# Kernel optimization log

Measured on AMD Instinct MI355X. Metric: run time of the kernel, lower is better.

Reference implementation:

```python
import jax, jax.numpy as jnp
import numpy as np

DIM = 384; KEY_DIM = 32; HEADS = 8; ATTN_RATIO = 4; RES = 14
D = ATTN_RATIO * KEY_DIM          # 128
DH = D * HEADS                    # 1024
QK = HEADS * KEY_DIM              # 256
B = 64
EPS = 1e-5
SCALE = KEY_DIM ** -0.5


def _bn(x, p):
    # inference-mode BatchNorm; p = [gamma, beta, mean, var] each [C]; channel axis = 1
    g, b, m, v = p
    shp = (1, -1) + (1,) * (x.ndim - 2)
    return (x - m.reshape(shp)) * jax.lax.rsqrt(v.reshape(shp) + EPS) * g.reshape(shp) + b.reshape(shp)


def _bn_params(k, c):
    k1, k2, k3, k4 = jax.random.split(k, 4)
    gamma = 1.0 + 0.1 * jax.random.normal(k1, (c,), dtype=jnp.float32)
    beta = 0.02 * jax.random.normal(k2, (c,), dtype=jnp.float32)
    mean = 0.1 * jax.random.normal(k3, (c,), dtype=jnp.float32)
    var = jax.random.uniform(k4, (c,), dtype=jnp.float32) + 0.5
    return jnp.stack([gamma, beta, mean, var])


def setup_inputs() -> dict:
    key = jax.random.key(0)
    ks = jax.random.split(key, 24)
    def rn(i, shape, s=0.05):
        return s * jax.random.normal(ks[i], shape, dtype=jnp.float32)
    # relative-position bias index table: offset (|dy|,|dx|) -> dy*RES+dx
    coords = np.stack(np.meshgrid(np.arange(RES), np.arange(RES), indexing='ij'), -1).reshape(-1, 2)
    off = np.abs(coords[:, None, :] - coords[None, :, :])  # [N,N,2]
    bias_idxs = jnp.asarray(off[..., 0] * RES + off[..., 1], dtype=jnp.int32)  # [N,N]
    return {
        'x': jax.random.normal(ks[0], (B, DIM, RES, RES), dtype=jnp.float32),
        'wq': rn(1, (QK, DIM)), 'bq': rn(2, (QK,)), 'bnq': _bn_params(ks[3], QK),
        'wk': rn(4, (QK, DIM)), 'bk': rn(5, (QK,)), 'bnk': _bn_params(ks[6], QK),
        'wv': rn(7, (DH, DIM)), 'bv': rn(8, (DH,)), 'bnv': _bn_params(ks[9], DH),
        'wvl': rn(10, (DH, 1, 3, 3)), 'bvl': rn(11, (DH,)), 'bnvl': _bn_params(ks[12], DH),
        'th1w': rn(13, (HEADS, HEADS), 0.2), 'th1b': rn(14, (HEADS,)),
        'th2w': rn(15, (HEADS, HEADS), 0.2), 'th2b': rn(16, (HEADS,)),
        'wp': rn(17, (DIM, DH)), 'bp': rn(18, (DIM,)), 'bnp': _bn_params(ks[19], DIM),
        'ab': rn(20, (HEADS, RES * RES), 0.1),
        'bias_idxs': bias_idxs,
    }


def reference(x, wq, bq, bnq, wk, bk, bnk, wv, bv, bnv, wvl, bvl, bnvl,
              th1w, th1b, th2w, th2b, wp, bp, bnp, ab, bias_idxs):
    Bn, C, H, W = x.shape
    N = H * W
    xf = x.reshape(Bn, C, N)
    # 1x1 conv + BN branches (channel GEMMs)
    q = _bn(jnp.einsum('oc,bcn->bon', wq, xf) + bq[None, :, None], bnq)
    k = _bn(jnp.einsum('oc,bcn->bon', wk, xf) + bk[None, :, None], bnk)
    v = _bn(jnp.einsum('oc,bcn->bon', wv, xf) + bv[None, :, None], bnv)  # [B,DH,N]
    # local value path: 3x3 depthwise conv + BN
    v_img = v.reshape(Bn, DH, H, W)
    v_local = jax.lax.conv_general_dilated(
        v_img, wvl, window_strides=(1, 1), padding='SAME',
        feature_group_count=DH, dimension_numbers=('NCHW', 'OIHW', 'NCHW'))
    v_local = _bn(v_local + bvl[None, :, None, None], bnvl)
    # attention
    qh = q.reshape(Bn, HEADS, KEY_DIM, N).transpose(0, 1, 3, 2)  # b h n d
    kh = k.reshape(Bn, HEADS, KEY_DIM, N)                        # b h d m
    vh = v.reshape(Bn, HEADS, D, N).transpose(0, 1, 3, 2)        # b h m e
    attn = jnp.einsum('bhnd,bhdm->bhnm', qh, kh) * SCALE
    attn = attn + ab[:, bias_idxs][None]                         # [1,H,N,N] positional bias
    attn = jnp.einsum('oh,bhnm->bonm', th1w, attn) + th1b[None, :, None, None]
    attn = jax.nn.softmax(attn, axis=-1)
    attn = jnp.einsum('oh,bhnm->bonm', th2w, attn) + th2b[None, :, None, None]
    out = jnp.einsum('bhnm,bhme->bhne', attn, vh)                # b h n e
    out = out.transpose(0, 1, 3, 2).reshape(Bn, DH, H, W) + v_local
    # proj: ReLU -> 1x1 conv -> BN
    out = jax.nn.relu(out)
    out = jnp.einsum('oc,bchw->bohw', wp, out) + bp[None, :, None, None]
    return _bn(out, bnp)
```

## Files before the change

### kernel.cpp

```cpp
#include <hip/hip_runtime.h>

#define B_     64
#define DIM_   384
#define RES_   14
#define N_     196
#define HEADS_ 8
#define KD_    32
#define D_     128
#define DH_    1024
#define QK_    256
#define CH_    1536
#define EPS_   1e-5f
#define SCALE_ 0.17677669529663687f

typedef unsigned short u16;
typedef unsigned int u32;
typedef short v8s __attribute__((ext_vector_type(8)));
typedef float v4f __attribute__((ext_vector_type(4)));
typedef u16  v4u __attribute__((ext_vector_type(4)));

static __device__ __forceinline__ u16 f2bf(float f) {
    unsigned int u = __builtin_bit_cast(unsigned int, f);
    u = (u + 0x7fffu + ((u >> 16) & 1u)) >> 16;
    return (u16)u;
}
static __device__ __forceinline__ float bf2f(u16 u) {
    unsigned int x = ((unsigned int)u) << 16;
    return __builtin_bit_cast(float, x);
}
static __device__ __forceinline__ u16 f2h(float f) {
    _Float16 h = (_Float16)f;
    return __builtin_bit_cast(u16, h);
}
static __device__ __forceinline__ float h2f(u16 u) {
    return (float)__builtin_bit_cast(_Float16, u);
}

#define WBI_OFF  0u
#define WPI_OFF  589824u
#define QI_OFF   983040u
#define KI_OFF   5177344u
#define VI_OFF   9371648u
#define VLOC_U16 53411840u
#define TAIL_OFF 79101952u
#define TB_OFF   98770944u
#define BIASE_OFF 98785920u

template<int KSTEPS>
static __device__ __forceinline__ void gemm_direct(
    const u16* __restrict__ Ag, const u16* __restrict__ Bg,
    v4f acc[4][4], int tid)
{
    const int lane = tid & 63, w = tid >> 6;
    const int wm = (w & 1) * 64, wn = (w >> 1) * 64;
    const int quad = lane >> 4, l16 = lane & 15;
    const u16* pa = Ag + quad * 1024 + (wm + l16) * 8;
    const u16* pb = Bg + quad * 1024 + (wn + l16) * 8;
    v8s a[2][4], b[2][4];
    #pragma unroll
    for (int i = 0; i < 4; i++) {
        a[0][i] = *(const v8s*)(pa + i * 128);
        b[0][i] = *(const v8s*)(pb + i * 128);
    }
    #pragma unroll
    for (int ks = 0; ks < KSTEPS; ks++) {
        const int cur = ks & 1, nxt = cur ^ 1;
        if (ks + 1 < KSTEPS) {
            const u16* qa = pa + (size_t)(ks + 1) * 4096;
            const u16* qb = pb + (size_t)(ks + 1) * 4096;
            #pragma unroll
            for (int i = 0; i < 4; i++) {
                a[nxt][i] = *(const v8s*)(qa + i * 128);
                b[nxt][i] = *(const v8s*)(qb + i * 128);
            }
        }
        #pragma unroll
        for (int i = 0; i < 4; i++)
            #pragma unroll
            for (int j = 0; j < 4; j++)
                acc[i][j] = __builtin_amdgcn_mfma_f32_16x16x32_bf16(a[cur][i], b[cur][j], acc[i][j], 0, 0, 0);
    }
}

template<int KSTEPS>
static __device__ __forceinline__ void gemm_direct3(
    const u16* __restrict__ Ag, const u16* __restrict__ Bg,
    v4f acc[4][4], int tid)
{
    const int lane = tid & 63, w = tid >> 6;
    const int wm = (w & 1) * 64, wn = (w >> 1) * 64;
    const int quad = lane >> 4, l16 = lane & 15;
    const u16* pa = Ag + quad * 1024 + (wm + l16) * 8;
    const u16* pb = Bg + quad * 1024 + (wn + l16) * 8;
    v8s a[3][4], b[3][4];
    #pragma unroll
    for (int s = 0; s < 2; s++) {
        #pragma unroll
        for (int i = 0; i < 4; i++) {
            a[s][i] = *(const v8s*)(pa + (size_t)s * 4096 + i * 128);
            b[s][i] = *(const v8s*)(pb + (size_t)s * 4096 + i * 128);
        }
    }
    #pragma unroll
    for (int ks = 0; ks < KSTEPS; ks++) {
        const int cur = ks % 3, nxt = (ks + 2) % 3;
        if (ks + 2 < KSTEPS) {
            const u16* qa = pa + (size_t)(ks + 2) * 4096;
            const u16* qb = pb + (size_t)(ks + 2) * 4096;
            #pragma unroll
            for (int i = 0; i < 4; i++) {
                a[nxt][i] = *(const v8s*)(qa + i * 128);
                b[nxt][i] = *(const v8s*)(qb + i * 128);
            }
        }
        #pragma unroll
        for (int i = 0; i < 4; i++)
            #pragma unroll
            for (int j = 0; j < 4; j++)
                acc[i][j] = __builtin_amdgcn_mfma_f32_16x16x32_bf16(a[cur][i], b[cur][j], acc[i][j], 0, 0, 0);
    }
}

__global__ __launch_bounds__(256) void k_pre(
    const float* __restrict__ x,
    const float* __restrict__ wq, const float* __restrict__ wk,
    const float* __restrict__ wv, const float* __restrict__ wp,
    const float* __restrict__ ab,
    const float* __restrict__ th1w, const float* __restrict__ th1b,
    const float* __restrict__ bq, const float* __restrict__ bnq,
    const float* __restrict__ bk, const float* __restrict__ bnk,
    const float* __restrict__ bv, const float* __restrict__ bnv,
    const float* __restrict__ bp, const float* __restrict__ bnp,
    const float* __restrict__ bvl, const float* __restrict__ bnvl,
    const int* __restrict__ bidx,
    u16* __restrict__ xI, u16* __restrict__ WbI, u16* __restrict__ WpI,
    float* __restrict__ TB, float* __restrict__ biasE)
{
    __shared__ float T[64][65];
    const int tid = threadIdx.x;
    if (blockIdx.x < 1536) {
        const int t  = blockIdx.x;
        const int n0 = (t & 3) * 64;
        const int k0 = ((t >> 2) % 6) * 64;
        const int b  = t / 24;
        const int c = tid & 63, r4 = tid >> 6;
        #pragma unroll
        for (int i = 0; i < 16; i++) {
            int kr = i * 4 + r4;
            int gn = n0 + c;
            T[kr][c] = (gn < N_) ? x[((size_t)b * DIM_ + k0 + kr) * N_ + gn] : 0.f;
        }
        __syncthreads();
        #pragma unroll
        for (int it = 0; it < 16; it++) {
            int j = it * 256 + tid;
            int kk = j & 63, nn = j >> 6;
            int k = k0 + kk, n = n0 + nn;
            xI[(size_t)b * 98304 + (n >> 7) * 49152 + (k >> 5) * 4096
               + ((k >> 3) & 3) * 1024 + (n & 127) * 8 + (k & 7)] = f2bf(T[kk][nn]);
        }
        return;
    }
    int i = (blockIdx.x - 1536) * 256 + tid;
    if (i < 589824) {
        int mt = i / 49152, rem = i % 49152;
        int ks = rem >> 12, r2 = rem & 4095;
        int q = r2 >> 10, row = (r2 >> 3) & 127, e = r2 & 7;
        int c = mt * 128 + row, k = ks * 32 + q * 8 + e;
        float v = (c < 256) ? wq[c * 384 + k]
                : (c < 512) ? wk[(c - 256) * 384 + k]
                            : wv[(size_t)(c - 512) * 384 + k];
        WbI[i] = f2bf(v);
    } else if (i < 983040) {
        int j = i - 589824;
        int mt = j >> 17, rem = j & 131071;
        int ks = rem >> 12, r2 = rem & 4095;
        int q = r2 >> 10, row = (r2 >> 3) & 127, e = r2 & 7;
        int p = mt * 128 + row, k = ks * 32 + q * 8 + e;
        WpI[j] = f2bf(wp[(size_t)p * 1024 + k]);
    } else if (i < 985984) {
        int j = i - 983040;
        if (j < 256) {
            int c = j;
            float s = bnq[c] * rsqrtf(bnq[768 + c] + EPS_);
            float t = (bq[c] - bnq[512 + c]) * s + bnq[256 + c];
            TB[c] = s * SCALE_; TB[256 + c] = t * SCALE_;
        } else if (j < 512) {
            int c = j - 256;
            float s = bnk[c] * rsqrtf(bnk[768 + c] + EPS_);
            float t = (bk[c] - bnk[512 + c]) * s + bnk[256 + c];
            TB[512 + c] = s; TB[768 + c] = t;
        } else if (j < 1536) {
            int c = j - 512;
            float s = bnv[c] * rsqrtf(bnv[3072 + c] + EPS_);
            float t = (bv[c] - bnv[2048 + c]) * s + bnv[1024 + c];
            TB[1024 + c] = s; TB[2048 + c] = t;
        } else if (j < 1920) {
            int c = j - 1536;
            float s = bnp[c] * rsqrtf(bnp[1152 + c] + EPS_);
            float t = (bp[c] - bnp[768 + c]) * s + bnp[384 + c];
            TB[3072 + c] = s; TB[3456 + c] = t;
        } else {
            int c = j - 1920;
            float s = bnvl[c] * rsqrtf(bnvl[3072 + c] + EPS_);
            float t = (bvl[c] - bnvl[2048 + c]) * s + bnvl[1024 + c];
            TB[3840 + c] = s; TB[4864 + c] = t;
        }
    } else if (i < 1293312) {
        int j = i - 985984;
        int m = j % N_;
        int t = j / N_;
        int o = t & 7;
        int n = t >> 3;
        int idx = bidx[n * N_ + m];
        float a = th1b[o];
        #pragma unroll
        for (int h = 0; h < 8; h++) a += th1w[o * 8 + h] * ab[h * N_ + idx];
        biasE[j] = a - 5.f;
    }
}

__global__ __launch_bounds__(256) void k_qkv(
    const u16* __restrict__ WbI, const u16* __restrict__ xI,
    const float* __restrict__ TB,
    u16* __restrict__ qI, u16* __restrict__ kI, u16* __restrict__ vI)
{
    const int tid = threadIdx.x;
    const int L = blockIdx.x + 2 * (blockIdx.y + 12 * blockIdx.z);
    const int idx = L >> 3;
    const int b  = (L & 7) * 8 + idx / 24;
    const int r  = idx % 24;
    const int mt = r >> 1, nt = r & 1;
    v4f acc[4][4] = {};
    gemm_direct<12>(WbI + (size_t)mt * 49152,
                    xI + ((size_t)b * 2 + nt) * 49152, acc, tid);

    const int lane = tid & 63, w = tid >> 6;
    const int wm = (w & 1) * 64, wn = (w >> 1) * 64;
    const int quad = lane >> 4, l16 = lane & 15;
    #pragma unroll
    for (int i = 0; i < 4; i++) {
        #pragma unroll
        for (int j = 0; j < 4; j++) {
            int gc = mt * 128 + wm + i * 16 + quad * 4;
            int n  = nt * 128 + wn + j * 16 + l16;
            v4f v = acc[i][j];
            if (gc < 256) {
                v4f s = *(const v4f*)&TB[gc];
                v4f t = *(const v4f*)&TB[256 + gc];
                v4u u;
                #pragma unroll
                for (int r2 = 0; r2 < 4; r2++) u[r2] = f2bf(v[r2] * s[r2] + t[r2]);
                *(v4u*)&qI[((size_t)(b * 8 + (gc >> 5)) * 256 + n) * 32 + (gc & 31)] = u;
            } else if (gc < 512) {
                int c = gc - 256;
                v4f s = *(const v4f*)&TB[512 + c];
                v4f t = *(const v4f*)&TB[768 + c];
                v4u u;
                #pragma unroll
                for (int r2 = 0; r2 < 4; r2++) u[r2] = f2bf(v[r2] * s[r2] + t[r2]);
                *(v4u*)&kI[((size_t)(b * 8 + (c >> 5)) * 256 + n) * 32 + (c & 31)] = u;
            } else {
                int c = gc - 512;
                if (n < 224) {
                    int o = c >> 7, e = c & 127;
                    u16* base = vI + ((size_t)(b * 8 + o) * 7 + (n >> 5)) * 4096
                                + ((n >> 3) & 3) * 1024 + (n & 7);
                    #pragma unroll
                    for (int r2 = 0; r2 < 4; r2++) {
                        u16 outv = 0;
                        if (n < N_) outv = f2bf(v[r2] * TB[1024 + c + r2] + TB[2048 + c + r2]);
                        base[(e + r2) * 8] = outv;
                    }
                }
            }
        }
    }
}

__global__ __launch_bounds__(256) void k_dwconv(
    const u16* __restrict__ vI, const float* __restrict__ wvl,
    const float* __restrict__ TB, u16* __restrict__ vlocI)
{
    __shared__ u16 V[64 * 230];
    const int tid = threadIdx.x;
    const int sub = blockIdx.x;
    const int b   = blockIdx.y;
    const int o   = sub >> 1;
    const int e0  = (sub & 1) * 64;
    const u16* img = vI + (size_t)(b * 8 + o) * 28672;

    {
        const int quad = tid >> 6, l = tid & 63;
        #pragma unroll
        for (int i = 0; i < 7; i++) {
            v8s u = *(const v8s*)&img[i * 4096 + quad * 1024 + (e0 + l) * 8];
            const u32* ui = (const u32*)&u;
            int m0 = i * 32 + quad * 8;
            u32* dst = (u32*)&V[l * 230 + m0];
            #pragma unroll
            for (int c = 0; c < 4; c++) dst[c] = ui[c];
        }
    }
    __syncthreads();

    const int e = tid & 63, j = tid >> 6;
    const int cg = sub * 64 + e;
    const int y0 = j * 4;
    const int ny = (j == 3) ? 2 : 4;
    float wgt[9];
    #pragma unroll
    for (int k = 0; k < 9; k++) wgt[k] = wvl[cg * 9 + k];
    const float sc = TB[3840 + cg], sh = TB[4864 + cg];
    u32 po[4][7];

    for (int yi = 0; yi < ny; yi++) {
        int y = y0 + yi;
        float a[3][16];
        #pragma unroll
        for (int dy = 0; dy < 3; dy++) {
            int yy = y + dy - 1;
            a[dy][0] = 0.f; a[dy][15] = 0.f;
            if (yy < 0 || yy > 13) {
                #pragma unroll
                for (int x = 1; x < 15; x++) a[dy][x] = 0.f;
            } else {
                const u16* rp = &V[e * 230 + yy * 14];
                #pragma unroll
                for (int c4 = 0; c4 < 7; c4++) {
                    u32 u = *(const u32*)&rp[c4 * 2];
                    a[dy][1 + 2 * c4] = bf2f((u16)(u & 0xffffu));
                    a[dy][2 + 2 * c4] = bf2f((u16)(u >> 16));
                }
            }
        }
        #pragma unroll
        for (int xp = 0; xp < 7; xp++) {
            u32 pk = 0;
            #pragma unroll
            for (int half = 0; half < 2; half++) {
                int x = 2 * xp + half;
                float s = 0.f;
                #pragma unroll
                for (int dy = 0; dy < 3; dy++)
                    #pragma unroll
                    for (int kx = 0; kx < 3; kx++)
                        s += wgt[dy * 3 + kx] * a[dy][x + kx];
                u16 bv = f2bf(s * sc + sh);
                pk |= ((u32)bv) << (16 * half);
            }
            po[yi][xp] = pk;
        }
    }
    __syncthreads();

    for (int yi = 0; yi < ny; yi++) {
        u32* dst = (u32*)&V[e * 196 + (y0 + yi) * 14];
        #pragma unroll
        for (int xp = 0; xp < 7; xp++) dst[xp] = po[yi][xp];
    }
    __syncthreads();

    for (int it = 0; it < 7; it++) {
        int idx = it * 256 + tid;
        if (idx < 1568) {
            int g = idx / 196, n = idx - g * 196;
            v4u lo, hi;
            #pragma unroll
            for (int r = 0; r < 4; r++) lo[r] = V[(g * 8 + r) * 196 + n];
            #pragma unroll
            for (int r = 0; r < 4; r++) hi[r] = V[(g * 8 + 4 + r) * 196 + n];
            u16* dst = vlocI + ((size_t)(b * 2 + (n >> 7)) * 32 + sub * 2 + (g >> 2)) * 4096
                     + (g & 3) * 1024 + (n & 127) * 8;
            *(v4u*)dst = lo;
            *(v4u*)(dst + 4) = hi;
        }
    }
}

__global__ __launch_bounds__(512) void k_attn_av(
    const u16* __restrict__ qI, const u16* __restrict__ kI,
    const u16* __restrict__ vI,
    const float* __restrict__ th1w,
    const float* __restrict__ th2w, const float* __restrict__ th2b,
    const float* __restrict__ biasE,
    const u16* __restrict__ vlocI, u16* __restrict__ aoI)
{
    __shared__ u16 Sl[8 * 16 * 228];
    __shared__ float red[128][4];
    __shared__ float invS[128];
    const int tid = threadIdx.x;
    const int w = tid >> 6, lane = tid & 63;
    const int quad = lane >> 4, l16 = lane & 15;
    const int L = blockIdx.x + 13 * blockIdx.y;
    const int idx = L >> 3;
    const int b  = (L & 7) * 8 + idx / 13;
    const int qt = idx % 13;
    const int n0 = qt * 16;

    {
        const int h = w;
        const u16* qb = qI + (size_t)(b * 8 + h) * 8192;
        const u16* kb = kI + (size_t)(b * 8 + h) * 8192;
        v8s qf = *(const v8s*)&qb[(n0 + l16) * 32 + quad * 8];
        #pragma unroll
        for (int mt = 0; mt < 13; mt++) {
            v8s kf = *(const v8s*)&kb[(mt * 16 + l16) * 32 + quad * 8];
            v4f acc = {};
            acc = __builtin_amdgcn_mfma_f32_16x16x32_bf16(kf, qf, acc, 0, 0, 0);
            v4u pk;
            #pragma unroll
            for (int r = 0; r < 4; r++) pk[r] = f2h(acc[r]);
            *(v4u*)&Sl[(h * 16 + l16) * 228 + mt * 16 + quad * 4] = pk;
        }
    }
    __syncthreads();

    const int mp  = (tid & 127) * 2;
    const int qh  = tid >> 7;
    const bool pvalid = (mp < N_);
    for (int qq = 0; qq < 4; qq++) {
        int q = qh * 4 + qq;
        int n = n0 + q;
        if (pvalid && n < N_) {
            const float* bE = biasE + (size_t)n * 1568 + mp;
            float S0[8], S1[8];
            #pragma unroll
            for (int h = 0; h < 8; h++) {
                u32 u = *(const u32*)&Sl[(h * 16 + q) * 228 + mp];
                S0[h] = h2f((u16)(u & 0xffffu));
                S1[h] = h2f((u16)(u >> 16));
            }
            u32 ew[8];
            #pragma unroll
            for (int o = 0; o < 8; o++) {
                float2 bb = *(const float2*)&bE[o * 196];
                float a0 = bb.x, a1 = bb.y;
                #pragma unroll
                for (int h = 0; h < 8; h++) {
                    a0 += th1w[o * 8 + h] * S0[h];
                    a1 += th1w[o * 8 + h] * S1[h];
                }
                ew[o] = (u32)f2h(__expf(a0)) | ((u32)f2h(__expf(a1)) << 16);
            }
            #pragma unroll
            for (int o = 0; o < 8; o++)
                *(u32*)&Sl[(o * 16 + q) * 228 + mp] = ew[o];
        }
    }
    __syncthreads();

    {
        int r = tid >> 2, quarter = tid & 3;
        int mstart = quarter * 48;
        int cnt = (quarter == 3) ? 26 : 24;
        const u16* rowp = &Sl[r * 228 + mstart];
        float s = 0.f;
        for (int i = 0; i < cnt; i++) {
            u32 u = *(const u32*)&rowp[i * 2];
            s += h2f((u16)(u & 0xffffu)) + h2f((u16)(u >> 16));
        }
        red[r][quarter] = s;
    }
    __syncthreads();
    if (tid < 128)
        invS[tid] = 1.f / (red[tid][0] + red[tid][1] + red[tid][2] + red[tid][3]);
    __syncthreads();

    for (int qq = 0; qq < 4; qq++) {
        int q = qh * 4 + qq;
        bool valid = pvalid && (n0 + q < N_);
        u32 pw[8];
        if (valid) {
            float s0[8], s1[8];
            #pragma unroll
            for (int h = 0; h < 8; h++) {
                u32 u = *(const u32*)&Sl[(h * 16 + q) * 228 + mp];
                float is = invS[h * 16 + q];
                s0[h] = h2f((u16)(u & 0xffffu)) * is;
                s1[h] = h2f((u16)(u >> 16)) * is;
            }
            #pragma unroll
            for (int o = 0; o < 8; o++) {
                float v0 = th2b[o], v1 = th2b[o];
                #pragma unroll
                for (int h = 0; h < 8; h++) {
                    v0 += th2w[o * 8 + h] * s0[h];
                    v1 += th2w[o * 8 + h] * s1[h];
                }
                pw[o] = (u32)f2bf(v0) | ((u32)f2bf(v1) << 16);
            }
        } else {
            #pragma unroll
            for (int o = 0; o < 8; o++) pw[o] = 0;
        }
        if (mp < 224) {
            #pragma unroll
            for (int o = 0; o < 8; o++)
                *(u32*)&Sl[(o * 16 + q) * 228 + mp] = pw[o];
        }
    }
    __syncthreads();

    {
        const int half_ = n0 >> 7;
        const int row0 = n0 & 127;
        const int n = n0 + l16;
        const bool act = (n < N_);
        const int o = w;
        const u16* vb = vI + (size_t)(b * 8 + o) * 28672;
        const u16* prow = &Sl[(o * 16 + l16) * 228];
        __builtin_amdgcn_s_setprio(1);
        #pragma unroll
        for (int eh = 0; eh < 2; eh++) {
            v4f acc[4] = {};
            v8s a[2][4];
            const u16* ab0 = vb + quad * 1024 + (eh * 64 + l16) * 8;
            #pragma unroll
            for (int e = 0; e < 4; e++) a[0][e] = *(const v8s*)(ab0 + e * 128);
            #pragma unroll
            for (int ks = 0; ks < 7; ks++) {
                const int cur = ks & 1, nxt = cur ^ 1;
                if (ks < 6) {
                    const u16* an = ab0 + (size_t)(ks + 1) * 4096;
                    #pragma unroll
                    for (int e = 0; e < 4; e++) a[nxt][e] = *(const v8s*)(an + e * 128);
                }
                v8s bfr = *(const v8s*)&prow[ks * 32 + quad * 8];
                #pragma unroll
                for (int e = 0; e < 4; e++)
                    acc[e] = __builtin_amdgcn_mfma_f32_16x16x32_bf16(a[cur][e], bfr, acc[e], 0, 0, 0);
            }
            if (act) {
                #pragma unroll
                for (int e = 0; e < 4; e++) {
                    const int c0 = o * 128 + (eh * 4 + e) * 16 + quad * 4;
                    const size_t ioff = ((size_t)(b * 2 + half_) * 32 + (c0 >> 5)) * 4096
                                      + ((c0 >> 3) & 3) * 1024 + (size_t)(row0 + l16) * 8 + (c0 & 7);
                    v4u lv = *(const v4u*)&vlocI[ioff];
                    v4u u;
                    #pragma unroll
                    for (int r = 0; r < 4; r++)
                        u[r] = f2bf(fmaxf(acc[e][r] + bf2f(lv[r]), 0.f));
                    *(v4u*)&aoI[ioff] = u;
                }
            }
        }
        __builtin_amdgcn_s_setprio(0);
    }
}

__global__ __launch_bounds__(256) void k_proj(
    const u16* __restrict__ WpI, const u16* __restrict__ aoI,
    const float* __restrict__ TB, float* __restrict__ out)
{
    const int tid = threadIdx.x;
    const int L = blockIdx.x + 2 * (blockIdx.y + 3 * blockIdx.z);
    const int idx = L >> 3;
    const int b  = (L & 7) * 8 + idx / 6;
    const int r  = idx % 6;
    const int mt = r >> 1, nt = r & 1;
    v4f acc[4][4] = {};
    gemm_direct3<32>(WpI + (size_t)mt * 131072,
                     aoI + ((size_t)b * 2 + nt) * 131072, acc, tid);

    const int lane = tid & 63, w = tid >> 6;
    const int wm = (w & 1) * 64, wn = (w >> 1) * 64;
    const int quad = lane >> 4, l16 = lane & 15;
    #pragma unroll
    for (int i = 0; i < 4; i++) {
        #pragma unroll
        for (int j = 0; j < 4; j++) {
            int p0 = mt * 128 + wm + i * 16 + quad * 4;
            int n  = nt * 128 + wn + j * 16 + l16;
            if (n < N_) {
                v4f s = *(const v4f*)&TB[3072 + p0];
                v4f t = *(const v4f*)&TB[3456 + p0];
                #pragma unroll
                for (int r2 = 0; r2 < 4; r2++)
                    out[((size_t)b * DIM_ + p0 + r2) * N_ + n] = acc[i][j][r2] * s[r2] + t[r2];
            }
        }
    }
}

extern "C" void kernel_launch(void* const* d_in, const int* in_sizes, int n_in,
                              void* d_out, int out_size, void* d_ws, size_t ws_size,
                              hipStream_t stream)
{
    const float* x    = (const float*)d_in[0];
    const float* wq   = (const float*)d_in[1];
    const float* bq   = (const float*)d_in[2];
    const float* bnq  = (const float*)d_in[3];
    const float* wk   = (const float*)d_in[4];
    const float* bk   = (const float*)d_in[5];
    const float* bnk  = (const float*)d_in[6];
    const float* wv   = (const float*)d_in[7];
    const float* bv   = (const float*)d_in[8];
    const float* bnv  = (const float*)d_in[9];
    const float* wvl  = (const float*)d_in[10];
    const float* bvl  = (const float*)d_in[11];
    const float* bnvl = (const float*)d_in[12];
    const float* th1w = (const float*)d_in[13];
    const float* th1b = (const float*)d_in[14];
    const float* th2w = (const float*)d_in[15];
    const float* th2b = (const float*)d_in[16];
    const float* wp   = (const float*)d_in[17];
    const float* bp   = (const float*)d_in[18];
    const float* bnp  = (const float*)d_in[19];
    const float* ab   = (const float*)d_in[20];
    const int*   bidx = (const int*)d_in[21];
    float* out = (float*)d_out;

    u16* wsb  = (u16*)d_ws;
    u16* WbI  = wsb + WBI_OFF;
    u16* WpI  = wsb + WPI_OFF;
    u16* qI   = wsb + QI_OFF;
    u16* kI   = wsb + KI_OFF;
    u16* vI   = wsb + VI_OFF;
    u16* vlocI = wsb + VLOC_U16;
    u16* xI   = wsb + TAIL_OFF;
    u16* aoI  = wsb + TAIL_OFF;
    float* TB    = (float*)(wsb + TB_OFF);
    float* biasE = (float*)(wsb + BIASE_OFF);

    k_pre<<<dim3(6588), 256, 0, stream>>>(x, wq, wk, wv, wp, ab, th1w, th1b,
                                          bq, bnq, bk, bnk, bv, bnv, bp, bnp, bvl, bnvl,
                                          bidx, xI, WbI, WpI, TB, biasE);
    k_qkv<<<dim3(2, 12, B_), 256, 0, stream>>>(WbI, xI, TB, qI, kI, vI);
    k_dwconv<<<dim3(16, B_), 256, 0, stream>>>(vI, wvl, TB, vlocI);
    k_attn_av<<<dim3(13, B_), 512, 0, stream>>>(qI, kI, vI, th1w, th2w, th2b,
                                                biasE, vlocI, aoI);
    k_proj<<<dim3(2, 3, B_), 256, 0, stream>>>(WpI, aoI, TB, out);
}
```

Before: 251.6 us.

## Keep attention scores in registers across head-mixing and softmax in attn kernel

Restructures the attention+AV kernel so each wave owns key tiles rather than heads. It computes all 8 heads' QK scores in registers, applies the th1 mix and exp there, and reduces row sums with shuffles plus a small shared buffer. The large shared score buffer and its multiple LDS round trips disappear. The th2-mixed probabilities are then staged per output head through a double-buffered small LDS tile, feeding a smaller per-wave AV MFMA. This raises register pressure, adds a barrier per head iteration, and moves the normalization into fp16 multiplies.

```diff
diff --git a/kernel.cpp b/kernel.cpp
--- a/kernel.cpp
+++ b/kernel.cpp
@@ -18,6 +18,8 @@
 typedef short v8s __attribute__((ext_vector_type(8)));
 typedef float v4f __attribute__((ext_vector_type(4)));
 typedef u16  v4u __attribute__((ext_vector_type(4)));
+typedef u32  v2u __attribute__((ext_vector_type(2)));
+typedef _Float16 h2 __attribute__((ext_vector_type(2)));
 
 static __device__ __forceinline__ u16 f2bf(float f) {
     unsigned int u = __builtin_bit_cast(unsigned int, f);
@@ -27,13 +29,6 @@
 static __device__ __forceinline__ float bf2f(u16 u) {
     unsigned int x = ((unsigned int)u) << 16;
     return __builtin_bit_cast(float, x);
-}
-static __device__ __forceinline__ u16 f2h(float f) {
-    _Float16 h = (_Float16)f;
-    return __builtin_bit_cast(u16, h);
-}
-static __device__ __forceinline__ float h2f(u16 u) {
-    return (float)__builtin_bit_cast(_Float16, u);
 }
 
 #define WBI_OFF  0u
@@ -378,7 +373,8 @@
     }
 }
 
-__global__ __launch_bounds__(512) void k_attn_av(
+#define SLST 232
+__global__ __launch_bounds__(512, 4) void k_attn_av(
     const u16* __restrict__ qI, const u16* __restrict__ kI,
     const u16* __restrict__ vI,
     const float* __restrict__ th1w,
@@ -386,9 +382,10 @@
     const float* __restrict__ biasE,
     const u16* __restrict__ vlocI, u16* __restrict__ aoI)
 {
-    __shared__ u16 Sl[8 * 16 * 228];
-    __shared__ float red[128][4];
-    __shared__ float invS[128];
+    __shared__ __attribute__((aligned(16))) u16 Ps[2][16 * SLST];
+    __shared__ float red[8][8][16];
+    __shared__ float invS[8][16];
+    __shared__ __attribute__((aligned(16))) u16 Zf[8];
     const int tid = threadIdx.x;
     const int w = tid >> 6, lane = tid & 63;
     const int quad = lane >> 4, l16 = lane & 15;
@@ -397,156 +394,140 @@
     const int b  = (L & 7) * 8 + idx / 13;
     const int qt = idx % 13;
     const int n0 = qt * 16;
+    if (tid < 8) Zf[tid] = 0;
+
+    const int nmt = (w < 5) ? 2 : 1;
+    const int nq  = n0 + l16;
+    const int nb  = (nq < N_) ? nq : 0;
+    const float* bErow = biasE + (size_t)nb * 1568;
+
+    h2 E[2][8][2] = {};
+    #pragma unroll
+    for (int mi = 0; mi < 2; mi++) {
+        if (mi >= nmt) break;
+        const int mt = w + mi * 8;
+        v4f S[8];
+        const u16* qb0 = qI + (size_t)b * 8 * 8192;
+        const u16* kb0 = kI + (size_t)b * 8 * 8192;
+        #pragma unroll
+        for (int h = 0; h < 8; h++) {
+            v8s qf = *(const v8s*)&qb0[h * 8192 + (n0 + l16) * 32 + quad * 8];
+            v8s kf = *(const v8s*)&kb0[h * 8192 + (mt * 16 + l16) * 32 + quad * 8];
+            v4f z = {};
+            S[h] = __builtin_amdgcn_mfma_f32_16x16x32_bf16(kf, qf, z, 0, 0, 0);
+        }
+        const bool mvalid = (mt < 12) || (quad == 0);
+        const int mb = mt * 16 + quad * 4;
+        if (mvalid) {
+            #pragma unroll
+            for (int o = 0; o < 8; o++) {
+                v4f a = *(const v4f*)&bErow[o * 196 + mb];
+                #pragma unroll
+                for (int h = 0; h < 8; h++) {
+                    float t1 = th1w[o * 8 + h];
+                    #pragma unroll
+                    for (int r = 0; r < 4; r++) a[r] += t1 * S[h][r];
+                }
+                E[mi][o][0] = h2{(_Float16)__expf(a[0]), (_Float16)__expf(a[1])};
+                E[mi][o][1] = h2{(_Float16)__expf(a[2]), (_Float16)__expf(a[3])};
+            }
+        }
+    }
 
     {
-        const int h = w;
-        const u16* qb = qI + (size_t)(b * 8 + h) * 8192;
-        const u16* kb = kI + (size_t)(b * 8 + h) * 8192;
-        v8s qf = *(const v8s*)&qb[(n0 + l16) * 32 + quad * 8];
-        #pragma unroll
-        for (int mt = 0; mt < 13; mt++) {
-            v8s kf = *(const v8s*)&kb[(mt * 16 + l16) * 32 + quad * 8];
-            v4f acc = {};
-            acc = __builtin_amdgcn_mfma_f32_16x16x32_bf16(kf, qf, acc, 0, 0, 0);
-            v4u pk;
-            #pragma unroll
-            for (int r = 0; r < 4; r++) pk[r] = f2h(acc[r]);
-            *(v4u*)&Sl[(h * 16 + l16) * 228 + mt * 16 + quad * 4] = pk;
-        }
+        float psum[8];
+        #pragma unroll
+        for (int o = 0; o < 8; o++) {
+            float s = (float)E[0][o][0].x + (float)E[0][o][0].y
+                    + (float)E[0][o][1].x + (float)E[0][o][1].y
+                    + (float)E[1][o][0].x + (float)E[1][o][0].y
+                    + (float)E[1][o][1].x + (float)E[1][o][1].y;
+            s += __shfl_xor(s, 16, 64);
+            s += __shfl_xor(s, 32, 64);
+            psum[o] = s;
+        }
+        red[w][quad * 2 + 0][l16] = psum[quad * 2 + 0];
+        red[w][quad * 2 + 1][l16] = psum[quad * 2 + 1];
     }
     __syncthreads();
-
-    const int mp  = (tid & 127) * 2;
-    const int qh  = tid >> 7;
-    const bool pvalid = (mp < N_);
-    for (int qq = 0; qq < 4; qq++) {
-        int q = qh * 4 + qq;
-        int n = n0 + q;
-        if (pvalid && n < N_) {
-            const float* bE = biasE + (size_t)n * 1568 + mp;
-            float S0[8], S1[8];
-            #pragma unroll
-            for (int h = 0; h < 8; h++) {
-                u32 u = *(const u32*)&Sl[(h * 16 + q) * 228 + mp];
-                S0[h] = h2f((u16)(u & 0xffffu));
-                S1[h] = h2f((u16)(u >> 16));
-            }
-            u32 ew[8];
-            #pragma unroll
-            for (int o = 0; o < 8; o++) {
-                float2 bb = *(const float2*)&bE[o * 196];
-                float a0 = bb.x, a1 = bb.y;
-                #pragma unroll
-                for (int h = 0; h < 8; h++) {
-                    a0 += th1w[o * 8 + h] * S0[h];
-                    a1 += th1w[o * 8 + h] * S1[h];
+    if (tid < 128) {
+        int o = tid >> 4, q = tid & 15;
+        float s = 0.f;
+        #pragma unroll
+        for (int wv = 0; wv < 8; wv++) s += red[wv][o][q];
+        invS[o][q] = 1.f / s;
+    }
+    __syncthreads();
+
+    #pragma unroll
+    for (int o = 0; o < 8; o++) {
+        float is = invS[o][l16];
+        h2 is2 = h2{(_Float16)is, (_Float16)is};
+        E[0][o][0] *= is2; E[0][o][1] *= is2;
+        E[1][o][0] *= is2; E[1][o][1] *= is2;
+    }
+
+    const int half_ = n0 >> 7;
+    const int row0 = n0 & 127;
+    const bool act = (nq < N_);
+    char* psrow0 = (char*)&Ps[0][0] + l16 * (SLST * 2);
+    char* psrow1 = (char*)&Ps[1][0] + l16 * (SLST * 2);
+
+    #pragma unroll
+    for (int o2 = 0; o2 < 8; o2++) {
+        char* psb = (o2 & 1) ? psrow1 : psrow0;
+        #pragma unroll
+        for (int mi = 0; mi < 2; mi++) {
+            if (mi >= nmt) break;
+            const int mt = w + mi * 8;
+            const bool mvalid = (mt < 12) || (quad == 0);
+            u32 pk0 = 0, pk1 = 0;
+            if (mvalid) {
+                float p0 = th2b[o2], p1 = th2b[o2], p2 = th2b[o2], p3 = th2b[o2];
+                #pragma unroll
+                for (int o = 0; o < 8; o++) {
+                    float wgt = th2w[o2 * 8 + o];
+                    p0 += wgt * (float)E[mi][o][0].x;
+                    p1 += wgt * (float)E[mi][o][0].y;
+                    p2 += wgt * (float)E[mi][o][1].x;
+                    p3 += wgt * (float)E[mi][o][1].y;
                 }
-                ew[o] = (u32)f2h(__expf(a0)) | ((u32)f2h(__expf(a1)) << 16);
-            }
-            #pragma unroll
-            for (int o = 0; o < 8; o++)
-                *(u32*)&Sl[(o * 16 + q) * 228 + mp] = ew[o];
-        }
-    }
-    __syncthreads();
-
-    {
-        int r = tid >> 2, quarter = tid & 3;
-        int mstart = quarter * 48;
-        int cnt = (quarter == 3) ? 26 : 24;
-        const u16* rowp = &Sl[r * 228 + mstart];
-        float s = 0.f;
-        for (int i = 0; i < cnt; i++) {
-            u32 u = *(const u32*)&rowp[i * 2];
-            s += h2f((u16)(u & 0xffffu)) + h2f((u16)(u >> 16));
-        }
-        red[r][quarter] = s;
-    }
-    __syncthreads();
-    if (tid < 128)
-        invS[tid] = 1.f / (red[tid][0] + red[tid][1] + red[tid][2] + red[tid][3]);
-    __syncthreads();
-
-    for (int qq = 0; qq < 4; qq++) {
-        int q = qh * 4 + qq;
-        bool valid = pvalid && (n0 + q < N_);
-        u32 pw[8];
-        if (valid) {
-            float s0[8], s1[8];
-            #pragma unroll
-            for (int h = 0; h < 8; h++) {
-                u32 u = *(const u32*)&Sl[(h * 16 + q) * 228 + mp];
-                float is = invS[h * 16 + q];
-                s0[h] = h2f((u16)(u & 0xffffu)) * is;
-                s1[h] = h2f((u16)(u >> 16)) * is;
-            }
-            #pragma unroll
-            for (int o = 0; o < 8; o++) {
-                float v0 = th2b[o], v1 = th2b[o];
-                #pragma unroll
-                for (int h = 0; h < 8; h++) {
-                    v0 += th2w[o * 8 + h] * s0[h];
-                    v1 += th2w[o * 8 + h] * s1[h];
-                }
-                pw[o] = (u32)f2bf(v0) | ((u32)f2bf(v1) << 16);
-            }
-        } else {
-            #pragma unroll
-            for (int o = 0; o < 8; o++) pw[o] = 0;
-        }
-        if (mp < 224) {
-            #pragma unroll
-            for (int o = 0; o < 8; o++)
-                *(u32*)&Sl[(o * 16 + q) * 228 + mp] = pw[o];
-        }
-    }
-    __syncthreads();
-
-    {
-        const int half_ = n0 >> 7;
-        const int row0 = n0 & 127;
-        const int n = n0 + l16;
-        const bool act = (n < N_);
-        const int o = w;
-        const u16* vb = vI + (size_t)(b * 8 + o) * 28672;
-        const u16* prow = &Sl[(o * 16 + l16) * 228];
+                pk0 = (u32)f2bf(p0) | ((u32)f2bf(p1) << 16);
+                pk1 = (u32)f2bf(p2) | ((u32)f2bf(p3) << 16);
+            }
+            v2u pw; pw[0] = pk0; pw[1] = pk1;
+            *(v2u*)(psb + mt * 32 + quad * 8) = pw;
+        }
+        const u16* vb = vI + (size_t)(b * 8 + o2) * 28672;
+        const u16* af = vb + quad * 1024 + (w * 16 + l16) * 8;
+        v8s va[7];
+        #pragma unroll
+        for (int ks = 0; ks < 7; ks++)
+            va[ks] = *(const v8s*)(af + (size_t)ks * 4096);
+        __syncthreads();
+
+        v4f acc = {};
         __builtin_amdgcn_s_setprio(1);
         #pragma unroll
-        for (int eh = 0; eh < 2; eh++) {
-            v4f acc[4] = {};
-            v8s a[2][4];
-            const u16* ab0 = vb + quad * 1024 + (eh * 64 + l16) * 8;
-            #pragma unroll
-            for (int e = 0; e < 4; e++) a[0][e] = *(const v8s*)(ab0 + e * 128);
-            #pragma unroll
-            for (int ks = 0; ks < 7; ks++) {
-                const int cur = ks & 1, nxt = cur ^ 1;
-                if (ks < 6) {
-                    const u16* an = ab0 + (size_t)(ks + 1) * 4096;
-                    #pragma unroll
-                    for (int e = 0; e < 4; e++) a[nxt][e] = *(const v8s*)(an + e * 128);
-                }
-                v8s bfr = *(const v8s*)&prow[ks * 32 + quad * 8];
-                #pragma unroll
-                for (int e = 0; e < 4; e++)
-                    acc[e] = __builtin_amdgcn_mfma_f32_16x16x32_bf16(a[cur][e], bfr, acc[e], 0, 0, 0);
-            }
-            if (act) {
-                #pragma unroll
-                for (int e = 0; e < 4; e++) {
-                    const int c0 = o * 128 + (eh * 4 + e) * 16 + quad * 4;
-                    const size_t ioff = ((size_t)(b * 2 + half_) * 32 + (c0 >> 5)) * 4096
-                                      + ((c0 >> 3) & 3) * 1024 + (size_t)(row0 + l16) * 8 + (c0 & 7);
-                    v4u lv = *(const v4u*)&vlocI[ioff];
-                    v4u u;
-                    #pragma unroll
-                    for (int r = 0; r < 4; r++)
-                        u[r] = f2bf(fmaxf(acc[e][r] + bf2f(lv[r]), 0.f));
-                    *(v4u*)&aoI[ioff] = u;
-                }
-            }
+        for (int ks = 0; ks < 7; ks++) {
+            v8s bfr = (ks == 6 && quad >= 2)
+                    ? *(const v8s*)&Zf[0]
+                    : *(const v8s*)(psb + ks * 64 + quad * 16);
+            acc = __builtin_amdgcn_mfma_f32_16x16x32_bf16(va[ks], bfr, acc, 0, 0, 0);
         }
         __builtin_amdgcn_s_setprio(0);
+
+        if (act) {
+            const int c0 = o2 * 128 + w * 16 + quad * 4;
+            const size_t ioff = ((size_t)(b * 2 + half_) * 32 + (c0 >> 5)) * 4096
+                              + ((c0 >> 3) & 3) * 1024 + (size_t)(row0 + l16) * 8 + (c0 & 7);
+            v4u lv = *(const v4u*)&vlocI[ioff];
+            v4u u;
+            #pragma unroll
+            for (int r = 0; r < 4; r++)
+                u[r] = f2bf(fmaxf(acc[r] + bf2f(lv[r]), 0.f));
+            *(v4u*)&aoI[ioff] = u;
+        }
     }
 }
 
```

Result: slower. 257.1 us (+2.2%).
